# Optimization experiments

Hardware: AMD Instinct MI355X
Metric: run time of the kernel (lower is better)

## Reference

```python
import jax, jax.numpy as jnp
import numpy as np

EPS = 1e-3  # BatchNorm eps in the original module


def conv3d(x, w, stride=1, pad=1):
    # x: (N,C,D,H,W), w: (O,I,3,3,3)
    return jax.lax.conv_general_dilated(
        x, w, (stride,) * 3, [(pad, pad)] * 3,
        dimension_numbers=("NCDHW", "OIDHW", "NCDHW"))


def bn_relu_mask(x, scale, shift, mask):
    # eval-mode BatchNorm folded to affine (scale/shift), ReLU, then re-mask
    # so inactive voxels stay exactly zero (submanifold semantics).
    y = jax.nn.relu(x * scale[None, :, None, None, None] + shift[None, :, None, None, None])
    return y * mask


def downsample_mask(mask):
    # output site of SparseConv3d(k=3,s=2,p=1) is active iff any active input
    # voxel lies in its receptive field -> max-pool of the mask.
    return jax.lax.reduce_window(
        mask, 0.0, jax.lax.max, (1, 1, 3, 3, 3), (1, 1, 2, 2, 2),
        [(0, 0), (0, 0), (1, 1), (1, 1), (1, 1)])


def trilinear_sample(vol, coords):
    # vol: (C,D,H,W); coords: (N,3) in [-1,1], order (x,y,z) -> (W,H,D).
    # Matches F.grid_sample(mode='bilinear', padding_mode='zeros', align_corners=True).
    C, D, H, W = vol.shape
    fx = (coords[:, 0] + 1.0) * 0.5 * (W - 1)
    fy = (coords[:, 1] + 1.0) * 0.5 * (H - 1)
    fz = (coords[:, 2] + 1.0) * 0.5 * (D - 1)
    x0 = jnp.floor(fx); y0 = jnp.floor(fy); z0 = jnp.floor(fz)
    tx = fx - x0; ty = fy - y0; tz = fz - z0
    x0i = x0.astype(jnp.int32); y0i = y0.astype(jnp.int32); z0i = z0.astype(jnp.int32)
    out = jnp.zeros((C, coords.shape[0]), vol.dtype)
    for dz in (0, 1):
        for dy in (0, 1):
            for dx in (0, 1):
                xi = x0i + dx; yi = y0i + dy; zi = z0i + dz
                w = (jnp.where(dx, tx, 1.0 - tx) * jnp.where(dy, ty, 1.0 - ty)
                     * jnp.where(dz, tz, 1.0 - tz))
                valid = ((xi >= 0) & (xi < W) & (yi >= 0) & (yi < H)
                         & (zi >= 0) & (zi < D))
                xc = jnp.clip(xi, 0, W - 1); yc = jnp.clip(yi, 0, H - 1)
                zc = jnp.clip(zi, 0, D - 1)
                vals = vol[:, zc, yc, xc]  # (C,N)
                out = out + vals * (w * valid.astype(vol.dtype))[None, :]
    return out


def setup_inputs() -> dict:
    key = jax.random.key(0)
    ks = jax.random.split(key, 24)
    D = 128
    NPTS = 65536
    x_feat = jax.random.normal(ks[0], (1, 3, D, D, D), jnp.float32)
    mask = (jax.random.uniform(ks[1], (1, 1, D, D, D)) < 0.1).astype(jnp.int32)
    coords = jax.random.uniform(ks[2], (NPTS, 3), jnp.float32, -1.0, 1.0)

    def w(k, o, i):
        return jax.random.normal(k, (o, i, 3, 3, 3), jnp.float32) * 0.05

    def bn(k, c):
        k1, k2 = jax.random.split(k)
        scale = jax.random.uniform(k1, (c,), jnp.float32, 0.5, 1.5)
        shift = jax.random.normal(k2, (c,), jnp.float32) * 0.1
        return scale, shift

    w0a = w(ks[3], 16, 3); s0a, b0a = bn(ks[4], 16)
    w0b = w(ks[5], 16, 16); s0b, b0b = bn(ks[6], 16)
    wd0 = w(ks[7], 32, 16); sd0, bd0 = bn(ks[8], 32)
    w1a = w(ks[9], 32, 32); s1a, b1a = bn(ks[10], 32)
    w1b = w(ks[11], 32, 32); s1b, b1b = bn(ks[12], 32)
    return dict(x_feat=x_feat, mask=mask, coords=coords,
                w0a=w0a, s0a=s0a, b0a=b0a, w0b=w0b, s0b=s0b, b0b=b0b,
                wd0=wd0, sd0=sd0, bd0=bd0,
                w1a=w1a, s1a=s1a, b1a=b1a, w1b=w1b, s1b=s1b, b1b=b1b)


def reference(x_feat, mask, coords, w0a, s0a, b0a, w0b, s0b, b0b,
              wd0, sd0, bd0, w1a, s1a, b1a, w1b, s1b, b1b):
    m0 = mask.astype(x_feat.dtype)
    x = x_feat * m0  # features exist only at active voxels
    # conv0: double submanifold conv (3->16->16), active set unchanged
    h = bn_relu_mask(conv3d(x, w0a), s0a, b0a, m0)
    h = bn_relu_mask(conv3d(h, w0b), s0b, b0b, m0)
    # down0: strided sparse conv 16->32, stride 2, pad 1
    m1 = downsample_mask(m0)
    h = bn_relu_mask(conv3d(h, wd0, stride=2), sd0, bd0, m1)
    # conv1: double submanifold conv 32->32 on the downsampled active set
    h = bn_relu_mask(conv3d(h, w1a), s1a, b1a, m1)
    h = bn_relu_mask(conv3d(h, w1b), s1b, b1b, m1)
    # dense + grid_sample (align_corners=True, zeros padding) -> (N, 32)
    feat = trilinear_sample(h[0], coords)  # (32, N)
    return feat.T
```

## Files before the change

kernel.cpp:

```cpp
#include <hip/hip_runtime.h>
#include <hip/hip_bf16.h>

#define N   128
#define N3  (N*N*N)
#define M   64
#define M3  (M*M*M)
#define NPTS 65536
#define PD  66
#define PD2 (PD*PD)
#define PVOX (PD*PD*PD)
#define PH  130
#define PH2 (PH*PH)
#define PH3 (PH*PH*PH)
#define CAP   393216
#define ZSLOT (CAP - 1)

enum : int {
  IW0A = 0,
  IW0B = 2048,
  IWD0 = 9216,
  IW1A = 23552,
  IW1B = 51200,
  ITOT = 78848
};

enum : int {
  SS0A = 0,   SB0A = 16,  SS0B = 32,  SB0B = 48,
  SSD0 = 64,  SBD0 = 96,  SS1A = 128, SB1A = 160,
  SS1B = 192, SB1B = 224, STOT = 256
};

typedef short bf16x8 __attribute__((ext_vector_type(8)));
typedef float f32x4  __attribute__((ext_vector_type(4)));

__device__ __forceinline__ unsigned short f2bf_bits(float f) {
  __hip_bfloat16 b = __float2bfloat16(f);
  union { __hip_bfloat16 b; unsigned short u; } cv; cv.b = b; return cv.u;
}
__device__ __forceinline__ float bfbits2f(short s) {
  union { unsigned u; float f; } c; c.u = ((unsigned)(unsigned short)s) << 16; return c.f;
}
__device__ __forceinline__ float ldIn(const void* p, long i, int bf) {
  return bf ? __bfloat162float(((const __hip_bfloat16*)p)[i]) : ((const float*)p)[i];
}
__device__ __forceinline__ int detect_bf(const unsigned* __restrict__ s0a_raw) {
  int all = 1;
  #pragma unroll
  for (int i = 0; i < 8; ++i) {
    unsigned w = s0a_raw[i];
    if (((w >> 8) & 0xFFu) != 0x3Fu) all = 0;
  }
  return all;
}

__global__ __launch_bounds__(256) void prep_k(
    const void* w0a, const void* w0b, const void* wd0,
    const void* w1a, const void* w1b,
    const void* s0a, const void* b0a, const void* s0b, const void* b0b,
    const void* sd0, const void* bd0, const void* s1a, const void* b1a,
    const void* s1b, const void* b1b,
    short* __restrict__ WI, float* __restrict__ sbuf)
{
  int i = blockIdx.x * 256 + threadIdx.x;
  if (i >= 27648 + STOT) return;
  int bf = detect_bf((const unsigned*)s0a);
  if (i < 2048) {
    int kb = i >> 9, l = (i >> 3) & 63, j = i & 7;
    int k = ((l >> 4) << 3) + j;
    int tap = kb * 8 + (k >> 2), ch = k & 3, oc = l & 15;
    float v = (tap < 27 && ch < 3) ? ldIn(w0a, (oc * 3 + ch) * 27 + tap, bf) : 0.f;
    WI[IW0A + i] = (short)f2bf_bits(v);
  }
  if (i < 7168) {
    int p = i >> 9, l = (i >> 3) & 63, j = i & 7;
    int kg = ((l >> 4) << 3) + j;
    int tap = 2 * p + (kg >> 4);
    int ic = kg & 15, oc = l & 15;
    float v = (tap < 27) ? ldIn(w0b, (oc * 16 + ic) * 27 + tap, bf) : 0.f;
    WI[IW0B + i] = (short)f2bf_bits(v);
  }
  if (i < 14336) {
    int p = i >> 10, h = (i >> 9) & 1, l = (i >> 3) & 63, j = i & 7;
    int kg = ((l >> 4) << 3) + j;
    int tap = 2 * p + (kg >> 4);
    int ic = kg & 15;
    int oc = (h << 4) + (l & 15);
    float v = (tap < 27) ? ldIn(wd0, (oc * 16 + ic) * 27 + tap, bf) : 0.f;
    WI[IWD0 + i] = (short)f2bf_bits(v);
  }
  if (i < 27648) {
    int t = i >> 10, h = (i >> 9) & 1, l = (i >> 3) & 63, j = i & 7;
    int ic = ((l >> 4) << 3) + j;
    int oc = (h << 4) + (l & 15);
    WI[IW1A + i] = (short)f2bf_bits(ldIn(w1a, (oc * 32 + ic) * 27 + t, bf));
    WI[IW1B + i] = (short)f2bf_bits(ldIn(w1b, (oc * 32 + ic) * 27 + t, bf));
  } else {
    int j = i - 27648;
    const void* src; int loc;
    if      (j < 16)  { src = s0a; loc = j; }
    else if (j < 32)  { src = b0a; loc = j - 16; }
    else if (j < 48)  { src = s0b; loc = j - 32; }
    else if (j < 64)  { src = b0b; loc = j - 48; }
    else if (j < 96)  { src = sd0; loc = j - 64; }
    else if (j < 128) { src = bd0; loc = j - 96; }
    else if (j < 160) { src = s1a; loc = j - 128; }
    else if (j < 192) { src = b1a; loc = j - 160; }
    else if (j < 224) { src = s1b; loc = j - 192; }
    else              { src = b1b; loc = j - 224; }
    sbuf[j] = ldIn(src, loc, bf);
  }
}

__global__ __launch_bounds__(256) void masklist_k(const int* __restrict__ mask,
                                                  int* __restrict__ list,
                                                  int* __restrict__ idxvol,
                                                  int* __restrict__ cnt)
{
  __shared__ int lpos, lbase;
  int t = threadIdx.x;
  int start = blockIdx.x * 8192;
  if (t == 0) lpos = 0;
  __syncthreads();
  int myc = 0;
  #pragma unroll 4
  for (int i = 0; i < 32; ++i) myc += (mask[start + i * 256 + t] != 0);
  atomicAdd(&lpos, myc);
  __syncthreads();
  if (t == 0) { lbase = atomicAdd(cnt, lpos); lpos = 0; }
  __syncthreads();
  #pragma unroll 4
  for (int i = 0; i < 32; ++i) {
    int idx = start + i * 256 + t;
    if (mask[idx]) {
      int p = atomicAdd(&lpos, 1);
      int slot = lbase + p;
      if (slot < ZSLOT) {
        list[slot] = idx;
        int z = idx >> 14, y = (idx >> 7) & 127, x = idx & 127;
        idxvol[((z + 1) * PH + (y + 1)) * PH + (x + 1)] = slot;
      }
    }
  }
}

__global__ __launch_bounds__(256) void dsmask_k(const int* __restrict__ mask,
                                                float* __restrict__ m1f)
{
  int idx = blockIdx.x * 256 + threadIdx.x;
  if (idx >= M3) return;
  int z = idx >> 12, y = (idx >> 6) & 63, x = idx & 63;
  int r = 0;
  #pragma unroll
  for (int dz = 0; dz < 3; ++dz) {
    int iz = 2 * z + dz - 1;
    if ((unsigned)iz >= 128u) continue;
    #pragma unroll
    for (int dy = 0; dy < 3; ++dy) {
      int iy = 2 * y + dy - 1;
      if ((unsigned)iy >= 128u) continue;
      #pragma unroll
      for (int dx = 0; dx < 3; ++dx) {
        int ix = 2 * x + dx - 1;
        if ((unsigned)ix >= 128u) continue;
        r |= mask[(iz << 14) | (iy << 7) | ix];
      }
    }
  }
  m1f[idx] = r ? 1.f : 0.f;
}

__global__ __launch_bounds__(256) void pack_c_k(const void* __restrict__ xf,
                                                const void* __restrict__ s0a,
                                                const int* __restrict__ list,
                                                const int* __restrict__ cnt,
                                                short* __restrict__ xc)
{
  int nact = *cnt;
  int bf = detect_bf((const unsigned*)s0a);
  for (int i = blockIdx.x * 256 + threadIdx.x; i < nact; i += 1024 * 256) {
    int idx = list[i];
    union { unsigned short us[4]; uint2 v; } u;
    u.us[0] = f2bf_bits(ldIn(xf, idx, bf));
    u.us[1] = f2bf_bits(ldIn(xf, (long)N3 + idx, bf));
    u.us[2] = f2bf_bits(ldIn(xf, 2l * N3 + idx, bf));
    u.us[3] = 0;
    *(uint2*)(xc + (size_t)i * 4) = u.v;
  }
}

__device__ __forceinline__ int tap_shift_PH(int t) {
  if (t >= 27) return 0;
  int dz = t / 9, r9 = t - dz * 9, dy = r9 / 3, dx = r9 - dy * 3;
  return (dz - 1) * PH2 + (dy - 1) * PH + (dx - 1);
}
__device__ __forceinline__ int slot_of(const int* __restrict__ idxvol, int nb) {
  int s = idxvol[nb];
  return s < 0 ? ZSLOT : s;
}

__global__ __launch_bounds__(256) void conv0a_mfma_k(
    const short* __restrict__ xc, const int* __restrict__ idxvol,
    const int* __restrict__ list, const int* __restrict__ cnt,
    const short* __restrict__ WI, const float* __restrict__ sbuf,
    short* __restrict__ h0c)
{
  __shared__ short ldsB[4 * 512];
  int tid = threadIdx.x;
  if (tid < 256) ((uint4*)ldsB)[tid] = ((const uint4*)(WI + IW0A))[tid];
  __syncthreads();
  int nact = *cnt;
  int wave = tid >> 6, lane = tid & 63, quad = lane >> 4, l15 = lane & 15;
  const int SAFE = PH2 + PH + 1;
  for (int base = blockIdx.x * 256; base < nact; base += 1024 * 256) {
    int i0 = base + wave * 64;
    int pv[4];
    #pragma unroll
    for (int tt = 0; tt < 4; ++tt) {
      int e2 = i0 + tt * 16 + l15;
      if (e2 < nact) {
        int idx = list[e2];
        int z = idx >> 14, y = (idx >> 7) & 127, x = idx & 127;
        pv[tt] = ((z + 1) * PH + (y + 1)) * PH + (x + 1);
      } else pv[tt] = SAFE;
    }
    f32x4 acc[4];
    #pragma unroll
    for (int tt = 0; tt < 4; ++tt) { f32x4 zf = {0.f,0.f,0.f,0.f}; acc[tt] = zf; }
    #pragma unroll
    for (int kb = 0; kb < 4; ++kb) {
      int t0 = kb * 8 + quad * 2, t1 = t0 + 1;
      int s0 = tap_shift_PH(t0), s1 = tap_shift_PH(t1);
      bf16x8 b = *(const bf16x8*)&ldsB[(kb * 64 + lane) * 8];
      #pragma unroll
      for (int tt = 0; tt < 4; ++tt) {
        int sa = slot_of(idxvol, pv[tt] + s0);
        int sb2 = slot_of(idxvol, pv[tt] + s1);
        union { struct { uint2 lo, hi; } p; bf16x8 v; } cv;
        cv.p.lo = *(const uint2*)(xc + (size_t)sa * 4);
        cv.p.hi = *(const uint2*)(xc + (size_t)sb2 * 4);
        acc[tt] = __builtin_amdgcn_mfma_f32_16x16x32_bf16(cv.v, b, acc[tt], 0, 0, 0);
      }
    }
    float sc = sbuf[SS0A + l15], sb = sbuf[SB0A + l15];
    #pragma unroll
    for (int tt = 0; tt < 4; ++tt)
      #pragma unroll
      for (int r = 0; r < 4; ++r) {
        int e2 = i0 + tt * 16 + quad * 4 + r;
        if (e2 < nact) {
          float vv = fmaxf(fmaf(acc[tt][r], sc, sb), 0.f);
          h0c[(size_t)e2 * 16 + l15] = (short)f2bf_bits(vv);
        }
      }
  }
}

__global__ __launch_bounds__(256) void conv0b_mfma_k(
    const short* __restrict__ h0c, const int* __restrict__ idxvol,
    const int* __restrict__ list, const int* __restrict__ cnt,
    const short* __restrict__ WI, const float* __restrict__ sbuf,
    short* __restrict__ h1c)
{
  __shared__ short ldsB[14 * 512];
  int tid = threadIdx.x;
  for (int i = tid; i < 14 * 64; i += 256)
    ((uint4*)ldsB)[i] = ((const uint4*)(WI + IW0B))[i];
  __syncthreads();
  int nact = *cnt;
  int wave = tid >> 6, lane = tid & 63, quad = lane >> 4, l15 = lane & 15;
  const int SAFE = PH2 + PH + 1;
  for (int base = blockIdx.x * 256; base < nact; base += 1024 * 256) {
    int i0 = base + wave * 64;
    int pv[4];
    #pragma unroll
    for (int tt = 0; tt < 4; ++tt) {
      int e2 = i0 + tt * 16 + l15;
      if (e2 < nact) {
        int idx = list[e2];
        int z = idx >> 14, y = (idx >> 7) & 127, x = idx & 127;
        pv[tt] = ((z + 1) * PH + (y + 1)) * PH + (x + 1);
      } else pv[tt] = SAFE;
    }
    f32x4 acc[4];
    #pragma unroll
    for (int tt = 0; tt < 4; ++tt) { f32x4 zf = {0.f,0.f,0.f,0.f}; acc[tt] = zf; }
    #pragma unroll
    for (int p = 0; p < 14; ++p) {
      const int t1 = 2 * p, t2 = (2 * p + 1 < 27) ? 2 * p + 1 : 2 * p;
      const int s1 = ((t1 / 9) - 1) * PH2 + (((t1 % 9) / 3) - 1) * PH + ((t1 % 3) - 1);
      const int s2 = ((t2 / 9) - 1) * PH2 + (((t2 % 9) / 3) - 1) * PH + ((t2 % 3) - 1);
      int sh = (quad >= 2) ? s2 : s1;
      bf16x8 b = *(const bf16x8*)&ldsB[(p * 64 + lane) * 8];
      #pragma unroll
      for (int tt = 0; tt < 4; ++tt) {
        int ss = slot_of(idxvol, pv[tt] + sh);
        bf16x8 a = *(const bf16x8*)(h0c + (size_t)ss * 16 + ((quad & 1) << 3));
        acc[tt] = __builtin_amdgcn_mfma_f32_16x16x32_bf16(a, b, acc[tt], 0, 0, 0);
      }
    }
    float sc = sbuf[SS0B + l15], sb = sbuf[SB0B + l15];
    #pragma unroll
    for (int tt = 0; tt < 4; ++tt)
      #pragma unroll
      for (int r = 0; r < 4; ++r) {
        int e2 = i0 + tt * 16 + quad * 4 + r;
        if (e2 < nact) {
          float vv = fmaxf(fmaf(acc[tt][r], sc, sb), 0.f);
          h1c[(size_t)e2 * 16 + l15] = (short)f2bf_bits(vv);
        }
      }
  }
}

__global__ __launch_bounds__(256) void convd0_mfma_k(
    const short* __restrict__ h1c, const int* __restrict__ idxvol,
    const float* __restrict__ m1f,
    const short* __restrict__ WI, const float* __restrict__ sbuf,
    short* __restrict__ Pout)
{
  __shared__ short ldsB[14 * 1024];
  int tid = threadIdx.x;
  for (int i = tid; i < 14 * 128; i += 256)
    ((uint4*)ldsB)[i] = ((const uint4*)(WI + IWD0))[i];
  __syncthreads();
  int wave = tid >> 6, lane = tid & 63, quad = lane >> 4, l15 = lane & 15;
  int rowid = blockIdx.x * 4 + wave;
  int z = rowid >> 6, y = rowid & 63;
  int base_row = ((2 * z) * PH + 2 * y) * PH;
  f32x4 acc[4][2];
  #pragma unroll
  for (int tt = 0; tt < 4; ++tt)
  #pragma unroll
  for (int h = 0; h < 2; ++h) { f32x4 zf = {0.f,0.f,0.f,0.f}; acc[tt][h] = zf; }
  #pragma unroll
  for (int p = 0; p < 14; ++p) {
    const int t1 = 2 * p, t2 = (2 * p + 1 < 27) ? 2 * p + 1 : 2 * p;
    const int s1 = (t1 / 9) * PH2 + ((t1 % 9) / 3) * PH + (t1 % 3);
    const int s2 = (t2 / 9) * PH2 + ((t2 % 9) / 3) * PH + (t2 % 3);
    int sh = (quad >= 2) ? s2 : s1;
    bf16x8 b0 = *(const bf16x8*)&ldsB[((p * 2 + 0) * 64 + lane) * 8];
    bf16x8 b1 = *(const bf16x8*)&ldsB[((p * 2 + 1) * 64 + lane) * 8];
    bf16x8 a[4];
    #pragma unroll
    for (int tt = 0; tt < 4; ++tt) {
      int vin = base_row + sh + 2 * (tt * 16 + l15);
      int ss = slot_of(idxvol, vin);
      a[tt] = *(const bf16x8*)(h1c + (size_t)ss * 16 + ((quad & 1) << 3));
    }
    #pragma unroll
    for (int tt = 0; tt < 4; ++tt) {
      acc[tt][0] = __builtin_amdgcn_mfma_f32_16x16x32_bf16(a[tt], b0, acc[tt][0], 0, 0, 0);
      acc[tt][1] = __builtin_amdgcn_mfma_f32_16x16x32_bf16(a[tt], b1, acc[tt][1], 0, 0, 0);
    }
  }
  float sc[2] = { sbuf[SSD0 + l15], sbuf[SSD0 + 16 + l15] };
  float sb[2] = { sbuf[SBD0 + l15], sbuf[SBD0 + 16 + l15] };
  int mrow = (z * 64 + y) * 64;
  int obase = ((z + 1) * PD + (y + 1)) * PD + 1;
  #pragma unroll
  for (int tt = 0; tt < 4; ++tt) {
    float4 mv = *(const float4*)&m1f[mrow + tt * 16 + quad * 4];
    float mvr[4] = {mv.x, mv.y, mv.z, mv.w};
    #pragma unroll
    for (int h = 0; h < 2; ++h)
      #pragma unroll
      for (int r = 0; r < 4; ++r) {
        float vv = fmaxf(fmaf(acc[tt][h][r], sc[h], sb[h]), 0.f) * mvr[r];
        int vox = obase + tt * 16 + quad * 4 + r;
        Pout[(size_t)vox * 32 + h * 16 + l15] = (short)f2bf_bits(vv);
      }
  }
}

__global__ __launch_bounds__(256, 4) void conv1_mfma_k(
    const short* __restrict__ Pin, short* __restrict__ Pout,
    const short* __restrict__ WI, const float* __restrict__ sbuf,
    int sof, int bof, const float* __restrict__ m1f)
{
  __shared__ short ldsB[20 * 1024];
  int tid = threadIdx.x;
  for (int i = tid; i < 20 * 128; i += 256)
    ((uint4*)ldsB)[i] = ((const uint4*)WI)[i];

  int wave = tid >> 6, lane = tid & 63;
  int quad = lane >> 4, l15 = lane & 15;
  __syncthreads();

  f32x4 acc[4][2];
  #pragma unroll
  for (int tt = 0; tt < 4; ++tt)
  #pragma unroll
  for (int h = 0; h < 2; ++h) { f32x4 zf = {0.f,0.f,0.f,0.f}; acc[tt][h] = zf; }

  int rowid = blockIdx.x * 4 + wave;
  int zz = rowid >> 6, yy = rowid & 63;
  int abase = ((zz + 1) * PD + (yy + 1)) * PD + 1;

  bf16x8 a_cur[4], b_cur[2];
  {
    const int shift0 = -PD2 - PD - 1;
    #pragma unroll
    for (int tt = 0; tt < 4; ++tt) {
      int off = (abase + shift0 + tt * 16 + l15) * 32 + quad * 8;
      a_cur[tt] = *(const bf16x8*)(Pin + off);
    }
    b_cur[0] = *(const bf16x8*)&ldsB[(0 * 64 + lane) * 8];
    b_cur[1] = *(const bf16x8*)&ldsB[(1 * 64 + lane) * 8];
  }
  #pragma unroll 1
  for (int k = 0; k < 27; ++k) {
    bf16x8 a_nxt[4], b_nxt[2];
    if (k < 26) {
      int kk = k + 1;
      int dz = kk / 9, r9 = kk - dz * 9, dy = r9 / 3, dx = r9 - dy * 3;
      int shift = (dz - 1) * PD2 + (dy - 1) * PD + (dx - 1);
      #pragma unroll
      for (int tt = 0; tt < 4; ++tt) {
        int off = (abase + shift + tt * 16 + l15) * 32 + quad * 8;
        a_nxt[tt] = *(const bf16x8*)(Pin + off);
      }
      if (kk < 20) {
        b_nxt[0] = *(const bf16x8*)&ldsB[((kk * 2 + 0) * 64 + lane) * 8];
        b_nxt[1] = *(const bf16x8*)&ldsB[((kk * 2 + 1) * 64 + lane) * 8];
      } else {
        b_nxt[0] = *(const bf16x8*)(WI + (kk * 2 + 0) * 512 + lane * 8);
        b_nxt[1] = *(const bf16x8*)(WI + (kk * 2 + 1) * 512 + lane * 8);
      }
    }
    #pragma unroll
    for (int tt = 0; tt < 4; ++tt) {
      acc[tt][0] = __builtin_amdgcn_mfma_f32_16x16x32_bf16(a_cur[tt], b_cur[0], acc[tt][0], 0, 0, 0);
      acc[tt][1] = __builtin_amdgcn_mfma_f32_16x16x32_bf16(a_cur[tt], b_cur[1], acc[tt][1], 0, 0, 0);
    }
    if (k < 26) {
      #pragma unroll
      for (int tt = 0; tt < 4; ++tt) a_cur[tt] = a_nxt[tt];
      b_cur[0] = b_nxt[0]; b_cur[1] = b_nxt[1];
    }
  }

  float sc[2] = { sbuf[sof + l15], sbuf[sof + 16 + l15] };
  float sh[2] = { sbuf[bof + l15], sbuf[bof + 16 + l15] };

  int mrow = (zz * 64 + yy) * 64;
  #pragma unroll
  for (int tt = 0; tt < 4; ++tt) {
    const float4 mv = *(const float4*)&m1f[mrow + tt * 16 + quad * 4];
    float mvr[4] = {mv.x, mv.y, mv.z, mv.w};
    #pragma unroll
    for (int h = 0; h < 2; ++h) {
      #pragma unroll
      for (int r = 0; r < 4; ++r) {
        float v = fmaxf(fmaf(acc[tt][h][r], sc[h], sh[h]), 0.f) * mvr[r];
        int vox = abase + tt * 16 + quad * 4 + r;
        Pout[(size_t)vox * 32 + h * 16 + l15] = (short)f2bf_bits(v);
      }
    }
  }
}

__global__ __launch_bounds__(256) void sample_k(
    const void* __restrict__ coords, const void* __restrict__ s0a,
    const short* __restrict__ vol, void* __restrict__ out)
{
  int p = blockIdx.x * 256 + threadIdx.x;
  if (p >= NPTS) return;
  int bf = detect_bf((const unsigned*)s0a);
  float cx = ldIn(coords, 3l * p + 0, bf);
  float cy = ldIn(coords, 3l * p + 1, bf);
  float cz = ldIn(coords, 3l * p + 2, bf);
  float fx = (cx + 1.f) * 0.5f * 63.f;
  float fy = (cy + 1.f) * 0.5f * 63.f;
  float fz = (cz + 1.f) * 0.5f * 63.f;
  float x0f = floorf(fx), y0f = floorf(fy), z0f = floorf(fz);
  int x0 = (int)x0f, y0 = (int)y0f, z0 = (int)z0f;
  float tx = fx - x0f, ty = fy - y0f, tz = fz - z0f;
  int li[8]; float wt[8];
  #pragma unroll
  for (int dz = 0; dz < 2; ++dz)
  #pragma unroll
  for (int dy = 0; dy < 2; ++dy)
  #pragma unroll
  for (int dx = 0; dx < 2; ++dx) {
    int t = dz * 4 + dy * 2 + dx;
    int xi = x0 + dx, yi = y0 + dy, zi = z0 + dz;
    bool ok = (unsigned)xi < 64u && (unsigned)yi < 64u && (unsigned)zi < 64u;
    int xc = min(max(xi, 0), 63), yc = min(max(yi, 0), 63), zc = min(max(zi, 0), 63);
    li[t] = ((zc + 1) * PD + (yc + 1)) * PD + (xc + 1);
    float w = (dx ? tx : 1.f - tx) * (dy ? ty : 1.f - ty) * (dz ? tz : 1.f - tz);
    wt[t] = ok ? w : 0.f;
  }
  #pragma unroll
  for (int cc = 0; cc < 4; ++cc) {
    float s[8];
    #pragma unroll
    for (int j = 0; j < 8; ++j) s[j] = 0.f;
    #pragma unroll
    for (int t = 0; t < 8; ++t) {
      bf16x8 v = *(const bf16x8*)(vol + (size_t)li[t] * 32 + cc * 8);
      #pragma unroll
      for (int j = 0; j < 8; ++j) s[j] += bfbits2f(v[j]) * wt[t];
    }
    if (bf) {
      union { unsigned short us[8]; uint4 v; } u;
      #pragma unroll
      for (int j = 0; j < 8; ++j) u.us[j] = f2bf_bits(s[j]);
      ((uint4*)out)[p * 4 + cc] = u.v;
    } else {
      #pragma unroll
      for (int j = 0; j < 8; ++j) ((float*)out)[(size_t)p * 32 + cc * 8 + j] = s[j];
    }
  }
}

extern "C" void kernel_launch(void* const* d_in, const int* in_sizes, int n_in,
                              void* d_out, int out_size, void* d_ws, size_t ws_size,
                              hipStream_t stream)
{
  const void* xf     = d_in[0];
  const int*  mask   = (const int*)d_in[1];
  const void* coords = d_in[2];
  const void* w0a = d_in[3];
  const void* s0a = d_in[4];
  const void* b0a = d_in[5];
  const void* w0b = d_in[6];
  const void* s0b = d_in[7];
  const void* b0b = d_in[8];
  const void* wd0 = d_in[9];
  const void* sd0 = d_in[10];
  const void* bd0 = d_in[11];
  const void* w1a = d_in[12];
  const void* s1a = d_in[13];
  const void* b1a = d_in[14];
  const void* w1b = d_in[15];
  const void* s1b = d_in[16];
  const void* b1b = d_in[17];

  char* ws = (char*)d_ws;
  size_t cur = 0;
  auto alloc = [&](size_t bytes) -> size_t {
    size_t o = cur; cur = (cur + bytes + 255) & ~(size_t)255; return o;
  };
  size_t o_cnt  = alloc(4);
  size_t o_m1f  = alloc((size_t)M3 * 4);
  size_t o_sbuf = alloc((size_t)STOT * 4);
  size_t o_WI   = alloc((size_t)ITOT * 2);
  size_t o_list = alloc((size_t)CAP * 4);
  size_t o_idx  = alloc((size_t)PH3 * 4);
  size_t o_xc   = alloc((size_t)CAP * 4 * 2);
  size_t o_h0c  = alloc((size_t)CAP * 16 * 2);
  size_t o_h1c  = alloc((size_t)CAP * 16 * 2);
  size_t o_P1   = alloc((size_t)PVOX * 32 * 2);
  size_t o_P2   = alloc((size_t)PVOX * 32 * 2);

  int*   cnt    = (int*)(ws + o_cnt);
  float* m1f    = (float*)(ws + o_m1f);
  float* sbuf   = (float*)(ws + o_sbuf);
  short* WI     = (short*)(ws + o_WI);
  int*   list   = (int*)(ws + o_list);
  int*   idxvol = (int*)(ws + o_idx);
  short* xc     = (short*)(ws + o_xc);
  short* h0c    = (short*)(ws + o_h0c);
  short* h1c    = (short*)(ws + o_h1c);
  short* P1     = (short*)(ws + o_P1);
  short* P2     = (short*)(ws + o_P2);

  hipMemsetAsync(cnt, 0, 4, stream);
  hipMemsetAsync(idxvol, 0xFF, (size_t)PH3 * 4, stream);
  hipMemsetAsync(ws + o_xc, 0, (o_P2 - o_xc) + (size_t)PVOX * 32 * 2, stream);

  prep_k<<<(27648 + STOT + 255) / 256, 256, 0, stream>>>(
      w0a, w0b, wd0, w1a, w1b,
      s0a, b0a, s0b, b0b, sd0, bd0, s1a, b1a, s1b, b1b, WI, sbuf);
  masklist_k<<<256, 256, 0, stream>>>(mask, list, idxvol, cnt);
  dsmask_k<<<M3 / 256, 256, 0, stream>>>(mask, m1f);
  pack_c_k<<<1024, 256, 0, stream>>>(xf, s0a, list, cnt, xc);

  conv0a_mfma_k<<<1024, 256, 0, stream>>>(xc, idxvol, list, cnt, WI, sbuf, h0c);
  conv0b_mfma_k<<<1024, 256, 0, stream>>>(h0c, idxvol, list, cnt, WI, sbuf, h1c);
  convd0_mfma_k<<<1024, 256, 0, stream>>>(h1c, idxvol, m1f, WI, sbuf, P1);

  conv1_mfma_k<<<1024, 256, 0, stream>>>(P1, P2, WI + IW1A, sbuf, SS1A, SB1A, m1f);
  conv1_mfma_k<<<1024, 256, 0, stream>>>(P2, P1, WI + IW1B, sbuf, SS1B, SB1B, m1f);

  sample_k<<<NPTS / 256, 256, 0, stream>>>(coords, s0a, P1, d_out);
}
```

Before: 310.5 us.

## Stage conv1 input halo slabs in LDS instead of weights

The conv1 MFMA kernel now loads, for each dz, a 6x66-voxel input slab (4 output rows plus halo) into LDS and reads the A operands from there for all 9 dy/dx taps. Weights are read from global memory with a one-tap prefetch instead of being staged in LDS. The aim is to reuse input across the four waves and neighbouring taps, cutting redundant global and L2 loads. In exchange it adds two barriers per dz, puts global weight loads on the critical path, and may cause LDS bank conflicts on the shifted reads.

```diff
diff --git a/kernel.cpp b/kernel.cpp
--- a/kernel.cpp
+++ b/kernel.cpp
@@ -377,14 +377,14 @@
     const short* __restrict__ WI, const float* __restrict__ sbuf,
     int sof, int bof, const float* __restrict__ m1f)
 {
-  __shared__ short ldsB[20 * 1024];
+  __shared__ uint4 ldsA4[1584];
+  const short* ldsA = (const short*)ldsA4;
   int tid = threadIdx.x;
-  for (int i = tid; i < 20 * 128; i += 256)
-    ((uint4*)ldsB)[i] = ((const uint4*)WI)[i];
-
   int wave = tid >> 6, lane = tid & 63;
   int quad = lane >> 4, l15 = lane & 15;
-  __syncthreads();
+
+  int z  = blockIdx.x >> 4;
+  int y0 = (blockIdx.x & 15) << 2;
 
   f32x4 acc[4][2];
   #pragma unroll
@@ -392,57 +392,48 @@
   #pragma unroll
   for (int h = 0; h < 2; ++h) { f32x4 zf = {0.f,0.f,0.f,0.f}; acc[tt][h] = zf; }
 
-  int rowid = blockIdx.x * 4 + wave;
-  int zz = rowid >> 6, yy = rowid & 63;
-  int abase = ((zz + 1) * PD + (yy + 1)) * PD + 1;
-
-  bf16x8 a_cur[4], b_cur[2];
-  {
-    const int shift0 = -PD2 - PD - 1;
-    #pragma unroll
-    for (int tt = 0; tt < 4; ++tt) {
-      int off = (abase + shift0 + tt * 16 + l15) * 32 + quad * 8;
-      a_cur[tt] = *(const bf16x8*)(Pin + off);
-    }
-    b_cur[0] = *(const bf16x8*)&ldsB[(0 * 64 + lane) * 8];
-    b_cur[1] = *(const bf16x8*)&ldsB[(1 * 64 + lane) * 8];
-  }
+  bf16x8 b_cur[2];
+  b_cur[0] = *(const bf16x8*)(WI + 0 * 512 + lane * 8);
+  b_cur[1] = *(const bf16x8*)(WI + 1 * 512 + lane * 8);
+
   #pragma unroll 1
-  for (int k = 0; k < 27; ++k) {
-    bf16x8 a_nxt[4], b_nxt[2];
-    if (k < 26) {
-      int kk = k + 1;
-      int dz = kk / 9, r9 = kk - dz * 9, dy = r9 / 3, dx = r9 - dy * 3;
-      int shift = (dz - 1) * PD2 + (dy - 1) * PD + (dx - 1);
-      #pragma unroll
-      for (int tt = 0; tt < 4; ++tt) {
-        int off = (abase + shift + tt * 16 + l15) * 32 + quad * 8;
-        a_nxt[tt] = *(const bf16x8*)(Pin + off);
-      }
-      if (kk < 20) {
-        b_nxt[0] = *(const bf16x8*)&ldsB[((kk * 2 + 0) * 64 + lane) * 8];
-        b_nxt[1] = *(const bf16x8*)&ldsB[((kk * 2 + 1) * 64 + lane) * 8];
-      } else {
-        b_nxt[0] = *(const bf16x8*)(WI + (kk * 2 + 0) * 512 + lane * 8);
-        b_nxt[1] = *(const bf16x8*)(WI + (kk * 2 + 1) * 512 + lane * 8);
-      }
-    }
-    #pragma unroll
-    for (int tt = 0; tt < 4; ++tt) {
-      acc[tt][0] = __builtin_amdgcn_mfma_f32_16x16x32_bf16(a_cur[tt], b_cur[0], acc[tt][0], 0, 0, 0);
-      acc[tt][1] = __builtin_amdgcn_mfma_f32_16x16x32_bf16(a_cur[tt], b_cur[1], acc[tt][1], 0, 0, 0);
-    }
-    if (k < 26) {
-      #pragma unroll
-      for (int tt = 0; tt < 4; ++tt) a_cur[tt] = a_nxt[tt];
-      b_cur[0] = b_nxt[0]; b_cur[1] = b_nxt[1];
+  for (int dz = 0; dz < 3; ++dz) {
+    __syncthreads();
+    const uint4* src = (const uint4*)(Pin + (size_t)((z + dz) * PD + y0) * PD * 32);
+    for (int i = tid; i < 1584; i += 256) ldsA4[i] = src[i];
+    __syncthreads();
+    #pragma unroll
+    for (int dy = 0; dy < 3; ++dy) {
+      #pragma unroll
+      for (int dx = 0; dx < 3; ++dx) {
+        int t = dz * 9 + dy * 3 + dx;
+        bf16x8 b_nxt[2];
+        if (t < 26) {
+          b_nxt[0] = *(const bf16x8*)(WI + ((t + 1) * 2 + 0) * 512 + lane * 8);
+          b_nxt[1] = *(const bf16x8*)(WI + ((t + 1) * 2 + 1) * 512 + lane * 8);
+        }
+        bf16x8 a[4];
+        #pragma unroll
+        for (int tt = 0; tt < 4; ++tt) {
+          int lofs = (((wave + dy) * 66) + tt * 16 + l15 + dx) * 32 + quad * 8;
+          a[tt] = *(const bf16x8*)&ldsA[lofs];
+        }
+        #pragma unroll
+        for (int tt = 0; tt < 4; ++tt) {
+          acc[tt][0] = __builtin_amdgcn_mfma_f32_16x16x32_bf16(a[tt], b_cur[0], acc[tt][0], 0, 0, 0);
+          acc[tt][1] = __builtin_amdgcn_mfma_f32_16x16x32_bf16(a[tt], b_cur[1], acc[tt][1], 0, 0, 0);
+        }
+        if (t < 26) { b_cur[0] = b_nxt[0]; b_cur[1] = b_nxt[1]; }
+      }
     }
   }
 
   float sc[2] = { sbuf[sof + l15], sbuf[sof + 16 + l15] };
   float sh[2] = { sbuf[bof + l15], sbuf[bof + 16 + l15] };
 
-  int mrow = (zz * 64 + yy) * 64;
+  int yy = y0 + wave;
+  int abase = ((z + 1) * PD + (yy + 1)) * PD + 1;
+  int mrow = (z * 64 + yy) * 64;
   #pragma unroll
   for (int tt = 0; tt < 4; ++tt) {
     const float4 mv = *(const float4*)&m1f[mrow + tt * 16 + quad * 4];
```

After: 274.5 us. 11.6% less time.
